# Kernel optimization log

Measured on AMD Instinct MI355X. Metric: run time of the kernel, lower is better.

## Reference

```python
import jax, jax.numpy as jnp
import numpy as np

# Model dims (match init_kwargs)
D_MODEL = 1024
D_INNER = 2048
D_STATE = 16
D_CONV = 4
DT_RANK = 64
H = 8                      # num_heads
P = D_INNER // H           # head_dim = 256
DT_MIN, DT_MAX = 1e-4, 1.0
BATCH, SEQ = 2, 4096
TOTAL_OUT = 2 * D_INNER + DT_RANK + 2 * H * D_STATE  # 4416 (no gated delta)
EPS = 1e-6


def _xavier(k, shape):
    fan_out, fan_in = shape
    return jax.random.normal(k, shape, jnp.float32) * np.sqrt(2.0 / (fan_in + fan_out))


def setup_inputs() -> dict:
    key = jax.random.key(0)
    ks = jax.random.split(key, 8)
    x = jax.random.normal(ks[0], (BATCH, SEQ, D_MODEL), jnp.float32)
    W_in = _xavier(ks[1], (TOTAL_OUT, D_MODEL))          # in_proj (no bias)
    W_dt = _xavier(ks[2], (H, DT_RANK))                  # dt_proj (no bias)
    conv_w = jax.random.normal(ks[3], (D_INNER, D_CONV), jnp.float32) * 0.1
    conv_b = jnp.zeros((D_INNER,), jnp.float32)
    # A_log init: log(1..d_state) per head
    A_log = jnp.broadcast_to(jnp.log(jnp.arange(1, D_STATE + 1, dtype=jnp.float32)), (H, D_STATE))
    Dskip = jnp.ones((H, P), jnp.float32)
    # dt_bias = inverse_softplus(dt), dt log-uniform in [dt_min, dt_max]
    dt0 = jnp.exp(jax.random.uniform(ks[4], (H,), jnp.float32)
                  * (np.log(DT_MAX) - np.log(DT_MIN)) + np.log(DT_MIN))
    dt_bias = dt0 + jnp.log(-jnp.expm1(-dt0))
    norm_w = jnp.ones((D_INNER,), jnp.float32)
    W_out = _xavier(ks[5], (D_MODEL, D_INNER))
    W_res = _xavier(ks[6], (D_INNER, D_MODEL))           # residual_proj (d_model != d_inner)
    return dict(x=x, W_in=W_in, W_dt=W_dt, conv_w=conv_w, conv_b=conv_b,
                A_log=A_log, Dskip=Dskip, dt_bias=dt_bias, norm_w=norm_w,
                W_out=W_out, W_res=W_res)


def _causal_dwconv(u, w, b):
    # u: (B,L,C) -> causal depthwise conv along L. w: (C,K), b: (C,)
    lhs = u.transpose(0, 2, 1)               # (B,C,L)
    rhs = w[:, None, :]                      # (C,1,K)
    out = jax.lax.conv_general_dilated(
        lhs, rhs, window_strides=(1,), padding=[(D_CONV - 1, 0)],
        dimension_numbers=('NCH', 'OIH', 'NCH'), feature_group_count=D_INNER)
    return (out + b[None, :, None]).transpose(0, 2, 1)


def reference(x, W_in, W_dt, conv_w, conv_b, A_log, Dskip, dt_bias, norm_w, W_out, W_res):
    Bsz, L, _ = x.shape
    p = x @ W_in.T                                            # (B,L,TOTAL_OUT)
    splits = np.cumsum([D_INNER, D_INNER, DT_RANK, H * D_STATE]).tolist()
    z, u, dt_h, Bf, Cf = jnp.split(p, splits, axis=-1)
    Bp = Bf.reshape(Bsz, L, H, D_STATE)
    Cp = Cf.reshape(Bsz, L, H, D_STATE)
    u = _causal_dwconv(u, conv_w, conv_b)                     # (B,L,D_INNER)
    # dt_prep: softplus(dt_raw + bias) clamped to [dt_min, dt_max]
    dt = jnp.clip(jax.nn.softplus(dt_h @ W_dt.T + dt_bias), DT_MIN, DT_MAX)  # (B,L,H)
    A = -jnp.exp(A_log)                                       # (H,N)
    uh = u.reshape(Bsz, L, H, P)

    def step(h, inp):
        u_t, dt_t, B_t, C_t = inp                             # (B,H,P),(B,H),(B,H,N),(B,H,N)
        dA = jnp.exp(dt_t[..., None] * A)                     # (B,H,N)
        h = h * dA[:, :, None, :] + (dt_t[:, :, None, None] * u_t[..., None]) * B_t[:, :, None, :]
        y_t = jnp.einsum('bhpn,bhn->bhp', h, C_t)
        return h, y_t

    h0 = jnp.zeros((Bsz, H, P, D_STATE), x.dtype)
    xs = (uh.transpose(1, 0, 2, 3), dt.transpose(1, 0, 2),
          Bp.transpose(1, 0, 2, 3), Cp.transpose(1, 0, 2, 3))
    _, ys = jax.lax.scan(step, h0, xs)                        # (L,B,H,P)
    y = ys.transpose(1, 0, 2, 3) + Dskip[None, None] * uh     # skip connection
    y = y.reshape(Bsz, L, D_INNER)

    residual_inner = x @ W_res.T                              # residual_proj
    # fused_out: g = RMSNorm(y * silu(z) + residual) * weight
    g = y * jax.nn.silu(z) + residual_inner
    g = g * jax.lax.rsqrt(jnp.mean(g * g, axis=-1, keepdims=True) + EPS) * norm_w
    return g @ W_out.T
```

## Files before the change

kernel.cpp:

```cpp
#include <hip/hip_runtime.h>
#include <hip/hip_bf16.h>
#include <math.h>

#define DMODEL  1024
#define DINNER  2048
#define DSTATE  16
#define DCONV   4
#define DTRANK  64
#define NH      8
#define PH      256
#define TOTOUT  4416
#define NPAD    4480
#define MB_ROWS 4096
#define LC      64
#define NCB     (MB_ROWS/LC)

typedef __attribute__((ext_vector_type(8))) short bf16x8;
typedef __attribute__((ext_vector_type(4))) float f32x4;

__device__ inline unsigned cvt2bf(float lo, float hi) {
    unsigned r;
    asm("v_cvt_pk_bf16_f32 %0, %1, %2" : "=v"(r) : "v"(lo), "v"(hi));
    return r;
}
__device__ inline ushort f2bf(float v) { return (ushort)(cvt2bf(v, v) & 0xffffu); }
__device__ inline float bf2f(ushort u) {
    union { unsigned u; float f; } w; w.u = (unsigned)u << 16; return w.f;
}
__device__ inline void gload16(const ushort* g, ushort* l) {
    __builtin_amdgcn_global_load_lds((const __attribute__((address_space(1))) unsigned*)(const void*)g,
                                     (__attribute__((address_space(3))) unsigned*)(void*)l, 16, 0, 0);
}

__global__ __launch_bounds__(256) void cvt_bf(const float* __restrict__ s,
                                              ushort* __restrict__ d) {
    size_t i = ((size_t)blockIdx.x * 256 + threadIdx.x) * 8;
    float4 v0 = *(const float4*)(s + i);
    float4 v1 = *(const float4*)(s + i + 4);
    uint4 o;
    o.x = cvt2bf(v0.x, v0.y); o.y = cvt2bf(v0.z, v0.w);
    o.z = cvt2bf(v1.x, v1.y); o.w = cvt2bf(v1.z, v1.w);
    *(uint4*)(d + i) = o;
}

__global__ __launch_bounds__(256) void cvt_weights(const float* __restrict__ W_in,
                                                   const float* __restrict__ W_res,
                                                   const float* __restrict__ W_out,
                                                   ushort* __restrict__ dst) {
    const size_t R0v = (size_t)TOTOUT * DMODEL;
    const size_t R0  = (size_t)NPAD * DMODEL;
    const size_t R1  = R0 + (size_t)DINNER * DMODEL;
    size_t i = ((size_t)blockIdx.x * 256 + threadIdx.x) * 8;
    float4 v0, v1;
    if (i < R0) {
        if (i < R0v) { v0 = *(const float4*)(W_in + i); v1 = *(const float4*)(W_in + i + 4); }
        else { v0 = make_float4(0.f,0.f,0.f,0.f); v1 = v0; }
    } else if (i < R1) {
        size_t o = i - R0; v0 = *(const float4*)(W_res + o); v1 = *(const float4*)(W_res + o + 4);
    } else {
        size_t o = i - R1; v0 = *(const float4*)(W_out + o); v1 = *(const float4*)(W_out + o + 4);
    }
    uint4 o;
    o.x = cvt2bf(v0.x, v0.y); o.y = cvt2bf(v0.z, v0.w);
    o.z = cvt2bf(v1.x, v1.y); o.w = cvt2bf(v1.z, v1.w);
    *(uint4*)(dst + i) = o;
}

template<int MODE>
__global__ __launch_bounds__(512) void gemm_p(const ushort* __restrict__ A,
                                              const ushort* __restrict__ W,
                                              float* __restrict__ C0,
                                              ushort* __restrict__ Cb,
                                              ushort* __restrict__ Zb,
                                              ushort* __restrict__ Ub,
                                              float* __restrict__ DBCp,
                                              int ntx, int K, int ldc) {
    __shared__ __align__(16) ushort L[3 * 12288];
    const int nwg  = gridDim.x;
    const int orig = blockIdx.x;
    const int swz  = (orig & 7) * (nwg >> 3) + (orig >> 3);
    const int bx = swz % ntx, by = swz / ntx;
    const int row0 = by * 256, col0 = bx * 128;

    const int t    = threadIdx.x;
    const int lane = t & 63, w = t >> 6;
    const int wr   = w >> 1, wc = w & 1;
    const int l15  = lane & 15, l4 = lane >> 4;

    const int r0g = t >> 2, s0g = t & 3;
    const int r1g = r0g + 128;
    const int rr0 = r0g ^ ((r0g >> 3) & 1), cc0 = s0g ^ ((r0g >> 1) & 3);
    const int rr1 = r1g ^ ((r1g >> 3) & 1), cc1 = s0g ^ ((r1g >> 1) & 3);
    const ushort* sA0 = A + (size_t)(row0 + rr0) * K + cc0 * 8;
    const ushort* sA1 = A + (size_t)(row0 + rr1) * K + cc1 * 8;
    const ushort* sB0 = W + (size_t)(col0 + rr0) * K + cc0 * 8;

    int offA[4], offB[4];
    #pragma unroll
    for (int mi = 0; mi < 4; mi++) {
        int r = wr * 64 + mi * 16 + l15;
        offA[mi] = (r * 32 + l4 * 8) ^ (((r >> 1) & 7) << 3);
    }
    #pragma unroll
    for (int ni = 0; ni < 4; ni++) {
        int r = wc * 64 + ni * 16 + l15;
        offB[ni] = 8192 + ((r * 32 + l4 * 8) ^ (((r >> 1) & 7) << 3));
    }

    f32x4 acc[4][4];
    #pragma unroll
    for (int i = 0; i < 4; i++)
        #pragma unroll
        for (int j = 0; j < 4; j++)
            acc[i][j] = (f32x4){0.f, 0.f, 0.f, 0.f};

    const int KT = K >> 5;
    {
        gload16(sA0,      &L[t * 8]);
        gload16(sA1,      &L[4096 + t * 8]);
        gload16(sB0,      &L[8192 + t * 8]);
        gload16(sA0 + 32, &L[12288 + t * 8]);
        gload16(sA1 + 32, &L[12288 + 4096 + t * 8]);
        gload16(sB0 + 32, &L[12288 + 8192 + t * 8]);
    }
    asm volatile("s_waitcnt vmcnt(3)" ::: "memory");
    __builtin_amdgcn_sched_barrier(0);
    __builtin_amdgcn_s_barrier();
    __builtin_amdgcn_sched_barrier(0);

    for (int kt = 0; kt < KT; ++kt) {
        const bool pre = (kt + 2) < KT;
        if (pre) {
            ushort* bp2 = &L[((kt + 2) % 3) * 12288];
            const int ko = (kt + 2) << 5;
            gload16(sA0 + ko, bp2 + t * 8);
            gload16(sA1 + ko, bp2 + 4096 + t * 8);
            gload16(sB0 + ko, bp2 + 8192 + t * 8);
        }
        const ushort* bp = &L[(kt % 3) * 12288];
        bf16x8 af[4], bw[4];
        #pragma unroll
        for (int mi = 0; mi < 4; mi++) af[mi] = *(const bf16x8*)(bp + offA[mi]);
        #pragma unroll
        for (int ni = 0; ni < 4; ni++) bw[ni] = *(const bf16x8*)(bp + offB[ni]);
        __builtin_amdgcn_s_setprio(1);
        #pragma unroll
        for (int mi = 0; mi < 4; mi++)
            #pragma unroll
            for (int ni = 0; ni < 4; ni++)
                acc[mi][ni] = __builtin_amdgcn_mfma_f32_16x16x32_bf16(af[mi], bw[ni], acc[mi][ni], 0, 0, 0);
        __builtin_amdgcn_s_setprio(0);
        if (pre) { asm volatile("s_waitcnt vmcnt(3)" ::: "memory"); }
        else     { asm volatile("s_waitcnt vmcnt(0)" ::: "memory"); }
        __builtin_amdgcn_sched_barrier(0);
        __builtin_amdgcn_s_barrier();
        __builtin_amdgcn_sched_barrier(0);
    }

    #pragma unroll
    for (int mi = 0; mi < 4; mi++) {
        #pragma unroll
        for (int ni = 0; ni < 4; ni++) {
            #pragma unroll
            for (int r = 0; r < 4; r++) {
                const int row = row0 + wr * 64 + mi * 16 + l4 * 4 + r;
                const int col = col0 + wc * 64 + ni * 16 + l15;
                const float v = acc[mi][ni][r];
                if (MODE == 0) {
                    C0[(size_t)row * ldc + col] = v;
                } else if (MODE == 1) {
                    size_t idx = (size_t)row * ldc + col;
                    Cb[idx] = f2bf(bf2f(Cb[idx]) + v);
                } else {
                    if (col0 < DINNER) {
                        Zb[(size_t)row * DINNER + col] = f2bf(v);
                    } else if (col0 < 2 * DINNER) {
                        Ub[(size_t)row * DINNER + (col - DINNER)] = f2bf(v);
                    } else if (col < TOTOUT) {
                        DBCp[(size_t)row * 320 + (col - 2 * DINNER)] = v;
                    }
                }
            }
        }
    }
}

__global__ __launch_bounds__(256) void dt_kernel(const float* __restrict__ DBC,
                                                 const float* __restrict__ W_dt,
                                                 const float* __restrict__ dt_bias,
                                                 const float* __restrict__ A_log,
                                                 float* __restrict__ dt,
                                                 float* __restrict__ dA) {
    int idx = blockIdx.x * blockDim.x + threadIdx.x;
    int h = idx % NH;
    int tr = idx / NH;
    const float* row = DBC + (size_t)tr * 320;
    float acc = dt_bias[h];
    #pragma unroll
    for (int r = 0; r < DTRANK; r++) acc = fmaf(row[r], W_dt[h * DTRANK + r], acc);
    float sp = acc > 20.f ? acc : log1pf(expf(acc));
    sp = fminf(fmaxf(sp, 1e-4f), 1.0f);
    dt[idx] = sp;
    #pragma unroll
    for (int n = 0; n < DSTATE; n++)
        dA[(size_t)idx * DSTATE + n] = expf(sp * (-expf(A_log[h * DSTATE + n])));
}

__global__ __launch_bounds__(256) void scan_local(const ushort* __restrict__ Ub,
                                                  const float* __restrict__ DBC,
                                                  const float* __restrict__ dt_,
                                                  const float* __restrict__ dA_,
                                                  const float* __restrict__ cw,
                                                  const float* __restrict__ cb,
                                                  float* __restrict__ hloc,
                                                  float* __restrict__ Pc) {
    const int c = blockIdx.x, h = blockIdx.y;
    const int pidx = threadIdx.x;
    const int ch = h * PH + pidx;
    const int t0 = c * LC;
    __shared__ float sdA[LC][DSTATE];
    __shared__ float sdB[LC][DSTATE];
    const int st = pidx >> 4, sn = pidx & 15;
    #pragma unroll
    for (int j = 0; j < 4; j++) {
        int tt = st + j * 16;
        size_t trow = (size_t)(t0 + tt);
        float dv = dt_[trow * NH + h];
        sdA[tt][sn] = dA_[(trow * NH + h) * DSTATE + sn];
        sdB[tt][sn] = dv * DBC[trow * 320 + 64 + h * DSTATE + sn];
    }
    const float w0 = cw[ch * 4], w1 = cw[ch * 4 + 1], w2 = cw[ch * 4 + 2], w3 = cw[ch * 4 + 3];
    const float bia = cb[ch];
    const int bs = (c / NCB) * MB_ROWS;
    float um3 = (t0 - 3 >= bs) ? bf2f(Ub[(size_t)(t0 - 3) * DINNER + ch]) : 0.f;
    float um2 = (t0 - 2 >= bs) ? bf2f(Ub[(size_t)(t0 - 2) * DINNER + ch]) : 0.f;
    float um1 = (t0 - 1 >= bs) ? bf2f(Ub[(size_t)(t0 - 1) * DINNER + ch]) : 0.f;
    __syncthreads();

    float hst[DSTATE] = {};
    for (int t = 0; t < LC; t++) {
        float u0 = bf2f(Ub[(size_t)(t0 + t) * DINNER + ch]);
        float up = fmaf(w3, u0, fmaf(w2, um1, fmaf(w1, um2, fmaf(w0, um3, bia))));
        um3 = um2; um2 = um1; um1 = u0;
        #pragma unroll
        for (int n = 0; n < DSTATE; n++)
            hst[n] = fmaf(hst[n], sdA[t][n], up * sdB[t][n]);
    }
    float* hl = hloc + (((size_t)c * NH + h) * PH + pidx) * DSTATE;
    #pragma unroll
    for (int n = 0; n < DSTATE; n++) hl[n] = hst[n];

    if (pidx < DSTATE) {
        float pr = 1.f;
        for (int t = 0; t < LC; t++) pr *= sdA[t][pidx];
        Pc[((size_t)c * NH + h) * DSTATE + pidx] = pr;
    }
}

__global__ __launch_bounds__(256) void scan_carry(const float* __restrict__ hloc,
                                                  const float* __restrict__ Pc,
                                                  float* __restrict__ Hent) {
    int g = blockIdx.x * 256 + threadIdx.x;
    int b = g >> 15;
    int r = g & 32767;
    int h = r >> 12;
    int inner = r & 4095;
    int n = r & 15;
    float carry = 0.f;
    for (int i = 0; i < NCB; i++) {
        int c = b * NCB + i;
        size_t idx = ((size_t)c * NH + h) * (PH * DSTATE) + inner;
        Hent[idx] = carry;
        carry = fmaf(Pc[((size_t)c * NH + h) * DSTATE + n], carry, hloc[idx]);
    }
}

__global__ __launch_bounds__(256) void scan_out(const ushort* __restrict__ Zb,
                                                const ushort* __restrict__ Ub,
                                                ushort* __restrict__ Yb,
                                                const float* __restrict__ DBC,
                                                const float* __restrict__ dt_,
                                                const float* __restrict__ dA_,
                                                const float* __restrict__ cw,
                                                const float* __restrict__ cb,
                                                const float* __restrict__ Dskip,
                                                const float* __restrict__ Hent) {
    const int c = blockIdx.x, h = blockIdx.y;
    const int pidx = threadIdx.x;
    const int ch = h * PH + pidx;
    const int t0 = c * LC;
    __shared__ float sdA[LC][DSTATE];
    __shared__ float sdB[LC][DSTATE];
    __shared__ float sC [LC][DSTATE];
    const int st = pidx >> 4, sn = pidx & 15;
    #pragma unroll
    for (int j = 0; j < 4; j++) {
        int tt = st + j * 16;
        size_t trow = (size_t)(t0 + tt);
        float dv = dt_[trow * NH + h];
        sdA[tt][sn] = dA_[(trow * NH + h) * DSTATE + sn];
        sdB[tt][sn] = dv * DBC[trow * 320 + 64 + h * DSTATE + sn];
        sC [tt][sn] =      DBC[trow * 320 + 192 + h * DSTATE + sn];
    }
    const float w0 = cw[ch * 4], w1 = cw[ch * 4 + 1], w2 = cw[ch * 4 + 2], w3 = cw[ch * 4 + 3];
    const float bia = cb[ch];
    const int bs = (c / NCB) * MB_ROWS;
    float um3 = (t0 - 3 >= bs) ? bf2f(Ub[(size_t)(t0 - 3) * DINNER + ch]) : 0.f;
    float um2 = (t0 - 2 >= bs) ? bf2f(Ub[(size_t)(t0 - 2) * DINNER + ch]) : 0.f;
    float um1 = (t0 - 1 >= bs) ? bf2f(Ub[(size_t)(t0 - 1) * DINNER + ch]) : 0.f;
    const float dsk = Dskip[ch];
    float hst[DSTATE];
    const float* he = Hent + (((size_t)c * NH + h) * PH + pidx) * DSTATE;
    #pragma unroll
    for (int n = 0; n < DSTATE; n++) hst[n] = he[n];
    __syncthreads();

    for (int t = 0; t < LC; t++) {
        size_t off = (size_t)(t0 + t) * DINNER + ch;
        float u0 = bf2f(Ub[off]);
        float up = fmaf(w3, u0, fmaf(w2, um1, fmaf(w1, um2, fmaf(w0, um3, bia))));
        um3 = um2; um2 = um1; um1 = u0;
        float a0 = 0.f, a1 = 0.f, a2 = 0.f, a3 = 0.f;
        #pragma unroll
        for (int n = 0; n < 4; n++) {
            hst[n +  0] = fmaf(hst[n +  0], sdA[t][n +  0], up * sdB[t][n +  0]);
            hst[n +  4] = fmaf(hst[n +  4], sdA[t][n +  4], up * sdB[t][n +  4]);
            hst[n +  8] = fmaf(hst[n +  8], sdA[t][n +  8], up * sdB[t][n +  8]);
            hst[n + 12] = fmaf(hst[n + 12], sdA[t][n + 12], up * sdB[t][n + 12]);
            a0 = fmaf(hst[n +  0], sC[t][n +  0], a0);
            a1 = fmaf(hst[n +  4], sC[t][n +  4], a1);
            a2 = fmaf(hst[n +  8], sC[t][n +  8], a2);
            a3 = fmaf(hst[n + 12], sC[t][n + 12], a3);
        }
        float yv = ((a0 + a1) + (a2 + a3)) + dsk * up;
        float zv = bf2f(Zb[off]);
        float sil = zv / (1.f + expf(-zv));
        Yb[off] = f2bf(yv * sil);
    }
}

__global__ __launch_bounds__(256) void rmsnorm_bf(const ushort* __restrict__ Yb,
                                                  const float* __restrict__ norm_w,
                                                  ushort* __restrict__ Gb) {
    const int row = blockIdx.x;
    const ushort* r = Yb + (size_t)row * DINNER;
    const int c0 = threadIdx.x * 8;
    uint4 packed = *(const uint4*)(r + c0);
    float v[8];
    v[0] = bf2f((ushort)(packed.x & 0xffff)); v[1] = bf2f((ushort)(packed.x >> 16));
    v[2] = bf2f((ushort)(packed.y & 0xffff)); v[3] = bf2f((ushort)(packed.y >> 16));
    v[4] = bf2f((ushort)(packed.z & 0xffff)); v[5] = bf2f((ushort)(packed.z >> 16));
    v[6] = bf2f((ushort)(packed.w & 0xffff)); v[7] = bf2f((ushort)(packed.w >> 16));
    float ss = 0.f;
    #pragma unroll
    for (int i = 0; i < 8; i++) ss = fmaf(v[i], v[i], ss);
    #pragma unroll
    for (int off = 32; off > 0; off >>= 1) ss += __shfl_down(ss, off);
    __shared__ float red[4];
    if ((threadIdx.x & 63) == 0) red[threadIdx.x >> 6] = ss;
    __syncthreads();
    float tot = red[0] + red[1] + red[2] + red[3];
    float inv = rsqrtf(tot / (float)DINNER + 1e-6f);
    float4 w0 = *(const float4*)(norm_w + c0);
    float4 w1 = *(const float4*)(norm_w + c0 + 4);
    uint4 o;
    o.x = cvt2bf(v[0] * inv * w0.x, v[1] * inv * w0.y);
    o.y = cvt2bf(v[2] * inv * w0.z, v[3] * inv * w0.w);
    o.z = cvt2bf(v[4] * inv * w1.x, v[5] * inv * w1.y);
    o.w = cvt2bf(v[6] * inv * w1.z, v[7] * inv * w1.w);
    *(uint4*)(Gb + (size_t)row * DINNER + c0) = o;
}

struct Lay {
    float *DBC, *DT, *DA, *PC, *HLOC, *HENT;
    ushort *YB, *ZB, *UB, *XBF, *WB;
    size_t total;
};
static Lay mk_layout(char* base, int Mr) {
    size_t o = 0;
    auto take = [&](size_t bytes) { char* p = base + o; o = (o + bytes + 255) & ~(size_t)255; return p; };
    Lay l;
    l.YB   = (ushort*)take((size_t)Mr * 2048 * 2);
    l.DBC  = (float*) take((size_t)Mr * 320 * 4);
    l.DT   = (float*) take((size_t)Mr * 8 * 4);
    l.DA   = (float*) take((size_t)Mr * 128 * 4);
    l.PC   = (float*) take((size_t)(Mr / 64) * NH * DSTATE * 4);
    l.HLOC = (float*) take((size_t)Mr * 512 * 4);
    l.HENT = (float*) take((size_t)Mr * 512 * 4);
    l.ZB   = (ushort*)take((size_t)Mr * 2048 * 2);
    l.UB   = (ushort*)take((size_t)Mr * 2048 * 2);
    l.XBF  = (ushort*)take((size_t)8192 * 1024 * 2);
    l.WB   = (ushort*)take(((size_t)NPAD * 1024 + (size_t)2048 * 1024 + (size_t)1024 * 2048) * 2);
    l.total = o;
    return l;
}

extern "C" void kernel_launch(void* const* d_in, const int* in_sizes, int n_in,
                              void* d_out, int out_size, void* d_ws, size_t ws_size,
                              hipStream_t stream) {
    const float* x       = (const float*)d_in[0];
    const float* W_in    = (const float*)d_in[1];
    const float* W_dt    = (const float*)d_in[2];
    const float* conv_w  = (const float*)d_in[3];
    const float* conv_b  = (const float*)d_in[4];
    const float* A_log   = (const float*)d_in[5];
    const float* Dskip   = (const float*)d_in[6];
    const float* dt_bias = (const float*)d_in[7];
    const float* norm_w  = (const float*)d_in[8];
    const float* W_out   = (const float*)d_in[9];
    const float* W_res   = (const float*)d_in[10];
    float* out = (float*)d_out;

    Lay probe = mk_layout(nullptr, 2 * MB_ROWS);
    const bool fat = ws_size >= probe.total;
    const int Mr = fat ? 2 * MB_ROWS : MB_ROWS;
    const int npass = fat ? 1 : 2;
    const int nbc = fat ? 2 : 1;
    Lay l = mk_layout((char*)d_ws, Mr);

    ushort* winb = l.WB;
    ushort* wrsb = winb + (size_t)NPAD * 1024;
    ushort* wotb = wrsb + (size_t)2048 * 1024;
    ushort* Gb   = l.ZB;

    cvt_weights<<<4288, 256, 0, stream>>>(W_in, W_res, W_out, l.WB);
    cvt_bf<<<(2 * MB_ROWS * DMODEL / 8) / 256, 256, 0, stream>>>(x, l.XBF);

    for (int b = 0; b < npass; b++) {
        const ushort* xb = l.XBF + (size_t)b * MB_ROWS * DMODEL;
        float* outb = out + (size_t)b * MB_ROWS * DMODEL;
        const int nty = Mr / 256;

        gemm_p<2><<<35 * nty, 512, 0, stream>>>(xb, winb, nullptr, nullptr, l.ZB, l.UB, l.DBC, 35, DMODEL, 0);
        dt_kernel<<<(Mr * NH) / 256, 256, 0, stream>>>(l.DBC, W_dt, dt_bias, A_log, l.DT, l.DA);
        scan_local<<<dim3(Mr / LC, NH), 256, 0, stream>>>(l.UB, l.DBC, l.DT, l.DA, conv_w, conv_b, l.HLOC, l.PC);
        scan_carry<<<nbc * 128, 256, 0, stream>>>(l.HLOC, l.PC, l.HENT);
        scan_out<<<dim3(Mr / LC, NH), 256, 0, stream>>>(l.ZB, l.UB, l.YB, l.DBC, l.DT, l.DA,
                                                        conv_w, conv_b, Dskip, l.HENT);
        gemm_p<1><<<16 * nty, 512, 0, stream>>>(xb, wrsb, nullptr, l.YB, nullptr, nullptr, nullptr, 16, DMODEL, DINNER);
        rmsnorm_bf<<<Mr, 256, 0, stream>>>(l.YB, norm_w, Gb);
        gemm_p<0><<<8 * nty, 512, 0, stream>>>(Gb, wotb, outb, nullptr, nullptr, nullptr, nullptr, 8, DINNER, DMODEL);
    }
}
```

Measured before the change: 307.5 us.

## Fuse residual projection into input GEMM with wider 256x256 tiles

Concatenates W_res after the padded W_in so the residual projection is computed in the same GEMM that reads x, removing a separate GEMM launch and its read-modify-write of Y. The big GEMM moves to 256x256 tiles with 8x4 MFMA accumulators per wave and larger LDS buffers to get more reuse. The residual is written to a new bf16 buffer and added in scan_out via fmaf. The cost is higher register and LDS pressure from the larger tile, plus an extra 16MB intermediate buffer in the workspace.

```diff
diff --git a/kernel.cpp b/kernel.cpp
--- a/kernel.cpp
+++ b/kernel.cpp
@@ -10,7 +10,8 @@
 #define NH      8
 #define PH      256
 #define TOTOUT  4416
-#define NPAD    4480
+#define NPAD    4608
+#define NTOT    6656
 #define MB_ROWS 4096
 #define LC      64
 #define NCB     (MB_ROWS/LC)
@@ -47,18 +48,18 @@
                                                    const float* __restrict__ W_res,
                                                    const float* __restrict__ W_out,
                                                    ushort* __restrict__ dst) {
-    const size_t R0v = (size_t)TOTOUT * DMODEL;
-    const size_t R0  = (size_t)NPAD * DMODEL;
-    const size_t R1  = R0 + (size_t)DINNER * DMODEL;
+    const size_t E0 = (size_t)TOTOUT * DMODEL;
+    const size_t E1 = (size_t)NPAD * DMODEL;
+    const size_t E2 = (size_t)NTOT * DMODEL;
     size_t i = ((size_t)blockIdx.x * 256 + threadIdx.x) * 8;
     float4 v0, v1;
-    if (i < R0) {
-        if (i < R0v) { v0 = *(const float4*)(W_in + i); v1 = *(const float4*)(W_in + i + 4); }
+    if (i < E1) {
+        if (i < E0) { v0 = *(const float4*)(W_in + i); v1 = *(const float4*)(W_in + i + 4); }
         else { v0 = make_float4(0.f,0.f,0.f,0.f); v1 = v0; }
-    } else if (i < R1) {
-        size_t o = i - R0; v0 = *(const float4*)(W_res + o); v1 = *(const float4*)(W_res + o + 4);
+    } else if (i < E2) {
+        size_t o = i - E1; v0 = *(const float4*)(W_res + o); v1 = *(const float4*)(W_res + o + 4);
     } else {
-        size_t o = i - R1; v0 = *(const float4*)(W_out + o); v1 = *(const float4*)(W_out + o + 4);
+        size_t o = i - E2; v0 = *(const float4*)(W_out + o); v1 = *(const float4*)(W_out + o + 4);
     }
     uint4 o;
     o.x = cvt2bf(v0.x, v0.y); o.y = cvt2bf(v0.z, v0.w);
@@ -66,25 +67,23 @@
     *(uint4*)(dst + i) = o;
 }
 
-template<int MODE>
-__global__ __launch_bounds__(512) void gemm_p(const ushort* __restrict__ A,
-                                              const ushort* __restrict__ W,
-                                              float* __restrict__ C0,
-                                              ushort* __restrict__ Cb,
-                                              ushort* __restrict__ Zb,
-                                              ushort* __restrict__ Ub,
-                                              float* __restrict__ DBCp,
-                                              int ntx, int K, int ldc) {
-    __shared__ __align__(16) ushort L[3 * 12288];
+__global__ __launch_bounds__(512, 2) void gemm_big(const ushort* __restrict__ A,
+                                                   const ushort* __restrict__ W,
+                                                   ushort* __restrict__ Zb,
+                                                   ushort* __restrict__ Ub,
+                                                   float* __restrict__ DBCp,
+                                                   ushort* __restrict__ RESb,
+                                                   int ntx, int K) {
+    __shared__ __align__(16) ushort L[3 * 16384];
     const int nwg  = gridDim.x;
     const int orig = blockIdx.x;
     const int swz  = (orig & 7) * (nwg >> 3) + (orig >> 3);
     const int bx = swz % ntx, by = swz / ntx;
-    const int row0 = by * 256, col0 = bx * 128;
+    const int row0 = by * 256, col0 = bx * 256;
 
     const int t    = threadIdx.x;
     const int lane = t & 63, w = t >> 6;
-    const int wr   = w >> 1, wc = w & 1;
+    const int wr   = w >> 2, wc = w & 3;
     const int l15  = lane & 15, l4 = lane >> 4;
 
     const int r0g = t >> 2, s0g = t & 3;
@@ -94,6 +93,118 @@
     const ushort* sA0 = A + (size_t)(row0 + rr0) * K + cc0 * 8;
     const ushort* sA1 = A + (size_t)(row0 + rr1) * K + cc1 * 8;
     const ushort* sB0 = W + (size_t)(col0 + rr0) * K + cc0 * 8;
+    const ushort* sB1 = W + (size_t)(col0 + rr1) * K + cc1 * 8;
+
+    int offA[8], offB[4];
+    #pragma unroll
+    for (int mi = 0; mi < 8; mi++) {
+        int r = wr * 128 + mi * 16 + l15;
+        offA[mi] = (r * 32 + l4 * 8) ^ (((r >> 1) & 7) << 3);
+    }
+    #pragma unroll
+    for (int ni = 0; ni < 4; ni++) {
+        int r = wc * 64 + ni * 16 + l15;
+        offB[ni] = 8192 + ((r * 32 + l4 * 8) ^ (((r >> 1) & 7) << 3));
+    }
+
+    f32x4 acc[8][4];
+    #pragma unroll
+    for (int i = 0; i < 8; i++)
+        #pragma unroll
+        for (int j = 0; j < 4; j++)
+            acc[i][j] = (f32x4){0.f, 0.f, 0.f, 0.f};
+
+    const int KT = K >> 5;
+    gload16(sA0,      &L[t * 8]);
+    gload16(sA1,      &L[4096 + t * 8]);
+    gload16(sB0,      &L[8192 + t * 8]);
+    gload16(sB1,      &L[12288 + t * 8]);
+    gload16(sA0 + 32, &L[16384 + t * 8]);
+    gload16(sA1 + 32, &L[16384 + 4096 + t * 8]);
+    gload16(sB0 + 32, &L[16384 + 8192 + t * 8]);
+    gload16(sB1 + 32, &L[16384 + 12288 + t * 8]);
+    asm volatile("s_waitcnt vmcnt(4)" ::: "memory");
+    __builtin_amdgcn_sched_barrier(0);
+    __builtin_amdgcn_s_barrier();
+    __builtin_amdgcn_sched_barrier(0);
+
+    for (int kt = 0; kt < KT; ++kt) {
+        const bool pre = (kt + 2) < KT;
+        if (pre) {
+            ushort* bp2 = &L[((kt + 2) % 3) * 16384];
+            const int ko = (kt + 2) << 5;
+            gload16(sA0 + ko, bp2 + t * 8);
+            gload16(sA1 + ko, bp2 + 4096 + t * 8);
+            gload16(sB0 + ko, bp2 + 8192 + t * 8);
+            gload16(sB1 + ko, bp2 + 12288 + t * 8);
+        }
+        const ushort* bp = &L[(kt % 3) * 16384];
+        bf16x8 af[8], bw[4];
+        #pragma unroll
+        for (int mi = 0; mi < 8; mi++) af[mi] = *(const bf16x8*)(bp + offA[mi]);
+        #pragma unroll
+        for (int ni = 0; ni < 4; ni++) bw[ni] = *(const bf16x8*)(bp + offB[ni]);
+        __builtin_amdgcn_s_setprio(1);
+        #pragma unroll
+        for (int mi = 0; mi < 8; mi++)
+            #pragma unroll
+            for (int ni = 0; ni < 4; ni++)
+                acc[mi][ni] = __builtin_amdgcn_mfma_f32_16x16x32_bf16(af[mi], bw[ni], acc[mi][ni], 0, 0, 0);
+        __builtin_amdgcn_s_setprio(0);
+        if (pre) { asm volatile("s_waitcnt vmcnt(4)" ::: "memory"); }
+        else     { asm volatile("s_waitcnt vmcnt(0)" ::: "memory"); }
+        __builtin_amdgcn_sched_barrier(0);
+        __builtin_amdgcn_s_barrier();
+        __builtin_amdgcn_sched_barrier(0);
+    }
+
+    #pragma unroll
+    for (int mi = 0; mi < 8; mi++) {
+        #pragma unroll
+        for (int ni = 0; ni < 4; ni++) {
+            #pragma unroll
+            for (int r = 0; r < 4; r++) {
+                const int row = row0 + wr * 128 + mi * 16 + l4 * 4 + r;
+                const int col = col0 + wc * 64 + ni * 16 + l15;
+                const float v = acc[mi][ni][r];
+                if (col0 < DINNER) {
+                    Zb[(size_t)row * DINNER + col] = f2bf(v);
+                } else if (col0 < 2 * DINNER) {
+                    Ub[(size_t)row * DINNER + (col - DINNER)] = f2bf(v);
+                } else if (col0 < NPAD) {
+                    if (col < TOTOUT)
+                        DBCp[(size_t)row * 320 + (col - 2 * DINNER)] = v;
+                } else {
+                    RESb[(size_t)row * DINNER + (col - NPAD)] = f2bf(v);
+                }
+            }
+        }
+    }
+}
+
+__global__ __launch_bounds__(512) void gemm_out(const ushort* __restrict__ A,
+                                                const ushort* __restrict__ W,
+                                                float* __restrict__ C0,
+                                                int ntx, int K, int ldc) {
+    __shared__ __align__(16) ushort L[3 * 12288];
+    const int nwg  = gridDim.x;
+    const int orig = blockIdx.x;
+    const int swz  = (orig & 7) * (nwg >> 3) + (orig >> 3);
+    const int bx = swz % ntx, by = swz / ntx;
+    const int row0 = by * 256, col0 = bx * 128;
+
+    const int t    = threadIdx.x;
+    const int lane = t & 63, w = t >> 6;
+    const int wr   = w >> 1, wc = w & 1;
+    const int l15  = lane & 15, l4 = lane >> 4;
+
+    const int r0g = t >> 2, s0g = t & 3;
+    const int r1g = r0g + 128;
+    const int rr0 = r0g ^ ((r0g >> 3) & 1), cc0 = s0g ^ ((r0g >> 1) & 3);
+    const int rr1 = r1g ^ ((r1g >> 3) & 1), cc1 = s0g ^ ((r1g >> 1) & 3);
+    const ushort* sA0 = A + (size_t)(row0 + rr0) * K + cc0 * 8;
+    const ushort* sA1 = A + (size_t)(row0 + rr1) * K + cc1 * 8;
+    const ushort* sB0 = W + (size_t)(col0 + rr0) * K + cc0 * 8;
 
     int offA[4], offB[4];
     #pragma unroll
@@ -115,14 +226,12 @@
             acc[i][j] = (f32x4){0.f, 0.f, 0.f, 0.f};
 
     const int KT = K >> 5;
-    {
-        gload16(sA0,      &L[t * 8]);
-        gload16(sA1,      &L[4096 + t * 8]);
-        gload16(sB0,      &L[8192 + t * 8]);
-        gload16(sA0 + 32, &L[12288 + t * 8]);
-        gload16(sA1 + 32, &L[12288 + 4096 + t * 8]);
-        gload16(sB0 + 32, &L[12288 + 8192 + t * 8]);
-    }
+    gload16(sA0,      &L[t * 8]);
+    gload16(sA1,      &L[4096 + t * 8]);
+    gload16(sB0,      &L[8192 + t * 8]);
+    gload16(sA0 + 32, &L[12288 + t * 8]);
+    gload16(sA1 + 32, &L[12288 + 4096 + t * 8]);
+    gload16(sB0 + 32, &L[12288 + 8192 + t * 8]);
     asm volatile("s_waitcnt vmcnt(3)" ::: "memory");
     __builtin_amdgcn_sched_barrier(0);
     __builtin_amdgcn_s_barrier();
@@ -158,31 +267,15 @@
     }
 
     #pragma unroll
-    for (int mi = 0; mi < 4; mi++) {
-        #pragma unroll
-        for (int ni = 0; ni < 4; ni++) {
+    for (int mi = 0; mi < 4; mi++)
+        #pragma unroll
+        for (int ni = 0; ni < 4; ni++)
             #pragma unroll
             for (int r = 0; r < 4; r++) {
                 const int row = row0 + wr * 64 + mi * 16 + l4 * 4 + r;
                 const int col = col0 + wc * 64 + ni * 16 + l15;
-                const float v = acc[mi][ni][r];
-                if (MODE == 0) {
-                    C0[(size_t)row * ldc + col] = v;
-                } else if (MODE == 1) {
-                    size_t idx = (size_t)row * ldc + col;
-                    Cb[idx] = f2bf(bf2f(Cb[idx]) + v);
-                } else {
-                    if (col0 < DINNER) {
-                        Zb[(size_t)row * DINNER + col] = f2bf(v);
-                    } else if (col0 < 2 * DINNER) {
-                        Ub[(size_t)row * DINNER + (col - DINNER)] = f2bf(v);
-                    } else if (col < TOTOUT) {
-                        DBCp[(size_t)row * 320 + (col - 2 * DINNER)] = v;
-                    }
-                }
+                C0[(size_t)row * ldc + col] = acc[mi][ni][r];
             }
-        }
-    }
 }
 
 __global__ __launch_bounds__(256) void dt_kernel(const float* __restrict__ DBC,
@@ -277,6 +370,7 @@
 
 __global__ __launch_bounds__(256) void scan_out(const ushort* __restrict__ Zb,
                                                 const ushort* __restrict__ Ub,
+                                                const ushort* __restrict__ RESb,
                                                 ushort* __restrict__ Yb,
                                                 const float* __restrict__ DBC,
                                                 const float* __restrict__ dt_,
@@ -335,7 +429,7 @@
         float yv = ((a0 + a1) + (a2 + a3)) + dsk * up;
         float zv = bf2f(Zb[off]);
         float sil = zv / (1.f + expf(-zv));
-        Yb[off] = f2bf(yv * sil);
+        Yb[off] = f2bf(fmaf(yv, sil, bf2f(RESb[off])));
     }
 }
 
@@ -373,7 +467,7 @@
 
 struct Lay {
     float *DBC, *DT, *DA, *PC, *HLOC, *HENT;
-    ushort *YB, *ZB, *UB, *XBF, *WB;
+    ushort *YB, *ZB, *UB, *RESB, *XBF, *WB;
     size_t total;
 };
 static Lay mk_layout(char* base, int Mr) {
@@ -389,8 +483,9 @@
     l.HENT = (float*) take((size_t)Mr * 512 * 4);
     l.ZB   = (ushort*)take((size_t)Mr * 2048 * 2);
     l.UB   = (ushort*)take((size_t)Mr * 2048 * 2);
+    l.RESB = (ushort*)take((size_t)Mr * 2048 * 2);
     l.XBF  = (ushort*)take((size_t)8192 * 1024 * 2);
-    l.WB   = (ushort*)take(((size_t)NPAD * 1024 + (size_t)2048 * 1024 + (size_t)1024 * 2048) * 2);
+    l.WB   = (ushort*)take(((size_t)NTOT * 1024 + (size_t)1024 * 2048) * 2);
     l.total = o;
     return l;
 }
@@ -418,12 +513,11 @@
     const int nbc = fat ? 2 : 1;
     Lay l = mk_layout((char*)d_ws, Mr);
 
-    ushort* winb = l.WB;
-    ushort* wrsb = winb + (size_t)NPAD * 1024;
-    ushort* wotb = wrsb + (size_t)2048 * 1024;
+    ushort* wcat = l.WB;
+    ushort* wotb = wcat + (size_t)NTOT * 1024;
     ushort* Gb   = l.ZB;
 
-    cvt_weights<<<4288, 256, 0, stream>>>(W_in, W_res, W_out, l.WB);
+    cvt_weights<<<((NTOT * 1024 + 2048 * 1024) / 8) / 256, 256, 0, stream>>>(W_in, W_res, W_out, l.WB);
     cvt_bf<<<(2 * MB_ROWS * DMODEL / 8) / 256, 256, 0, stream>>>(x, l.XBF);
 
     for (int b = 0; b < npass; b++) {
@@ -431,14 +525,13 @@
         float* outb = out + (size_t)b * MB_ROWS * DMODEL;
         const int nty = Mr / 256;
 
-        gemm_p<2><<<35 * nty, 512, 0, stream>>>(xb, winb, nullptr, nullptr, l.ZB, l.UB, l.DBC, 35, DMODEL, 0);
+        gemm_big<<<26 * nty, 512, 0, stream>>>(xb, wcat, l.ZB, l.UB, l.DBC, l.RESB, 26, DMODEL);
         dt_kernel<<<(Mr * NH) / 256, 256, 0, stream>>>(l.DBC, W_dt, dt_bias, A_log, l.DT, l.DA);
         scan_local<<<dim3(Mr / LC, NH), 256, 0, stream>>>(l.UB, l.DBC, l.DT, l.DA, conv_w, conv_b, l.HLOC, l.PC);
         scan_carry<<<nbc * 128, 256, 0, stream>>>(l.HLOC, l.PC, l.HENT);
-        scan_out<<<dim3(Mr / LC, NH), 256, 0, stream>>>(l.ZB, l.UB, l.YB, l.DBC, l.DT, l.DA,
+        scan_out<<<dim3(Mr / LC, NH), 256, 0, stream>>>(l.ZB, l.UB, l.RESB, l.YB, l.DBC, l.DT, l.DA,
                                                         conv_w, conv_b, Dskip, l.HENT);
-        gemm_p<1><<<16 * nty, 512, 0, stream>>>(xb, wrsb, nullptr, l.YB, nullptr, nullptr, nullptr, 16, DMODEL, DINNER);
         rmsnorm_bf<<<Mr, 256, 0, stream>>>(l.YB, norm_w, Gb);
-        gemm_p<0><<<8 * nty, 512, 0, stream>>>(Gb, wotb, outb, nullptr, nullptr, nullptr, nullptr, 8, DINNER, DMODEL);
-    }
-}
+        gemm_out<<<8 * nty, 512, 0, stream>>>(Gb, wotb, outb, 8, DINNER, DMODEL);
+    }
+}
```

Result: slower. 326.4 us (+6.1%).
